# Optimization experiments

Hardware: AMD Instinct MI355X
Metric: run time of the kernel (lower is better)

The kernel has to match this reference:

```python
import jax, jax.numpy as jnp
import numpy as np

DIM = 256
HEADS = 8
WS = 7
MLP_HIDDEN = int(DIM * 2.0)
LN_EPS = 1e-5


def _ln(x, g, b):
    m = x.mean(-1, keepdims=True)
    v = ((x - m) ** 2).mean(-1, keepdims=True)
    return (x - m) / jnp.sqrt(v + LN_EPS) * g + b


def setup_inputs() -> dict:
    key = jax.random.key(0)
    ks = jax.random.split(key, 6)
    B, H, W, C = 32, 56, 56, DIM
    s = lambda k, shape: jax.random.normal(k, shape, jnp.float32) * 0.02
    return {
        "x": jax.random.normal(ks[0], (B, H * W, C), jnp.float32),
        "H": H,
        "W": W,
        "norm1_g": jnp.ones((C,), jnp.float32),
        "norm1_b": jnp.zeros((C,), jnp.float32),
        "in_proj_w": s(ks[1], (3 * C, C)),
        "in_proj_b": jnp.zeros((3 * C,), jnp.float32),
        "out_proj_w": s(ks[2], (C, C)),
        "out_proj_b": jnp.zeros((C,), jnp.float32),
        "norm2_g": jnp.ones((C,), jnp.float32),
        "norm2_b": jnp.zeros((C,), jnp.float32),
        "mlp_w1": s(ks[3], (MLP_HIDDEN, C)),
        "mlp_b1": jnp.zeros((MLP_HIDDEN,), jnp.float32),
        "mlp_w2": s(ks[4], (C, MLP_HIDDEN)),
        "mlp_b2": jnp.zeros((C,), jnp.float32),
    }


def reference(x, H, W, norm1_g, norm1_b, in_proj_w, in_proj_b, out_proj_w,
              out_proj_b, norm2_g, norm2_b, mlp_w1, mlp_b1, mlp_w2, mlp_b2):
    B, N, C = x.shape
    ws = WS
    shortcut = x

    h = _ln(x, norm1_g, norm1_b).reshape(B, H, W, C)  # channels-last (equiv. math)
    pad_h = (ws - H % ws) % ws
    pad_w = (ws - W % ws) % ws
    h = jnp.pad(h, ((0, 0), (0, pad_h), (0, pad_w), (0, 0)), mode="reflect")
    Hp, Wp = H + pad_h, W + pad_w
    nh, nw = Hp // ws, Wp // ws

    # window partition -> (B*nh*nw, ws*ws, C)
    h = h.reshape(B, nh, ws, nw, ws, C).transpose(0, 1, 3, 2, 4, 5)
    h = h.reshape(B * nh * nw, ws * ws, C)

    # torch nn.MultiheadAttention (batch_first), q=k=v=h
    hd = C // HEADS
    qkv = h @ in_proj_w.T + in_proj_b               # (Bw, L, 3C)
    q, k, v = jnp.split(qkv, 3, axis=-1)
    Bw, L, _ = q.shape
    q = q.reshape(Bw, L, HEADS, hd).transpose(0, 2, 1, 3)
    k = k.reshape(Bw, L, HEADS, hd).transpose(0, 2, 1, 3)
    v = v.reshape(Bw, L, HEADS, hd).transpose(0, 2, 1, 3)
    scores = jnp.einsum("bhqd,bhkd->bhqk", q, k) / jnp.sqrt(jnp.float32(hd))
    attn = jax.nn.softmax(scores, axis=-1)
    o = jnp.einsum("bhqk,bhkd->bhqd", attn, v)
    o = o.transpose(0, 2, 1, 3).reshape(Bw, L, C)
    o = o @ out_proj_w.T + out_proj_b

    # window merge, crop padding
    o = o.reshape(B, nh, nw, ws, ws, C).transpose(0, 1, 3, 2, 4, 5)
    o = o.reshape(B, Hp, Wp, C)[:, :H, :W, :].reshape(B, N, C)

    x = shortcut + o
    h2 = _ln(x, norm2_g, norm2_b)
    h2 = jax.nn.gelu(h2 @ mlp_w1.T + mlp_b1, approximate=False) @ mlp_w2.T + mlp_b2
    return x + h2
```

## Files before the change

kernel.cpp:

```cpp
#include <hip/hip_runtime.h>
#include <hip/hip_bf16.h>
#include <math.h>

#define NTOK 3136
#define C_ 256
#define HEADS_ 8
#define HD 32
#define WS_ 7
#define L_ 49
#define NWIN 2048
#define NWH 16384
#define M_ 100352
#define MLPH 512
#define WHSZ 2048

typedef __bf16 bf16x8 __attribute__((ext_vector_type(8)));
typedef float f32x4 __attribute__((ext_vector_type(4)));

__device__ __forceinline__ unsigned short f2bf(float f) {
    union { float f; unsigned u; } v; v.f = f;
    unsigned r = v.u + 0x7fffu + ((v.u >> 16) & 1u);
    return (unsigned short)(r >> 16);
}
__device__ __forceinline__ float bf2f(unsigned short s) {
    union { unsigned u; float f; } v; v.u = ((unsigned)s) << 16;
    return v.f;
}

__device__ __forceinline__ int t2rr(int t) {
    int win = t / L_;
    int l   = t - win * L_;
    int b_  = win >> 6, wh = (win >> 3) & 7, ww = win & 7;
    int ld7 = l / WS_;
    int y   = wh * WS_ + ld7;
    int xc  = ww * WS_ + (l - ld7 * WS_);
    return b_ * NTOK + y * 56 + xc;
}

template <int NBN>
__device__ __forceinline__ void xcd_decode(int nb, int& bm, int& bn) {
    int h = blockIdx.x;
    int fid = (h & 7) * (nb >> 3) + (h >> 3);
    int bmi = fid / NBN;
    bm = bmi * 128;
    bn = (fid - bmi * NBN) * 128;
}

__global__ __launch_bounds__(256) void cvt_kernel(
    const float* __restrict__ in, unsigned short* __restrict__ out, int n)
{
    int i = blockIdx.x * 256 + threadIdx.x;
    if (i < n) out[i] = f2bf(in[i]);
}

__global__ __launch_bounds__(256) void ln_kernel(
    const float* __restrict__ x, const float* __restrict__ gamma,
    const float* __restrict__ beta, unsigned short* __restrict__ out)
{
    int wave = threadIdx.x >> 6;
    int lane = threadIdx.x & 63;
    int p = blockIdx.x * 4 + wave;
    const float* row = x + (size_t)p * C_;
    float4 v = *(const float4*)(row + lane * 4);
    float s  = v.x + v.y + v.z + v.w;
    float ss = v.x * v.x + v.y * v.y + v.z * v.z + v.w * v.w;
    #pragma unroll
    for (int m = 1; m < 64; m <<= 1) {
        s  += __shfl_xor(s, m, 64);
        ss += __shfl_xor(ss, m, 64);
    }
    float mean = s * (1.0f / C_);
    float var  = ss * (1.0f / C_) - mean * mean;
    float inv  = rsqrtf(var + 1e-5f);
    float4 gv = *(const float4*)(gamma + lane * 4);
    float4 bv = *(const float4*)(beta + lane * 4);
    int b_ = p / NTOK, n = p - b_ * NTOK;
    int y = n / 56, xc = n - y * 56;
    int win = (b_ * 8 + y / WS_) * 8 + xc / WS_;
    int l   = (y % WS_) * WS_ + (xc % WS_);
    size_t orow = (size_t)(win * L_ + l) * C_;
    unsigned short o[4];
    o[0] = f2bf((v.x - mean) * inv * gv.x + bv.x);
    o[1] = f2bf((v.y - mean) * inv * gv.y + bv.y);
    o[2] = f2bf((v.z - mean) * inv * gv.z + bv.z);
    o[3] = f2bf((v.w - mean) * inv * gv.w + bv.w);
    *(uint2*)(out + orow + lane * 4) = *(const uint2*)o;
}

#define GBK 32

__device__ __forceinline__ void gload_lds16(const void* g, void* l) {
    __builtin_amdgcn_global_load_lds(
        (const __attribute__((address_space(1))) unsigned*)g,
        (__attribute__((address_space(3))) unsigned*)l, 16, 0, 0);
}

__global__ __launch_bounds__(256) void mgemm_qkv(
    const unsigned short* __restrict__ A, const unsigned short* __restrict__ W,
    const float* __restrict__ bias, unsigned short* __restrict__ qkv)
{
    __shared__ __align__(16) unsigned short As[4096];
    __shared__ __align__(16) unsigned short Bs[4096];

    int tid  = threadIdx.x;
    int w    = tid >> 6;
    int lane = tid & 63;
    int wr = w >> 1, wc = w & 1;
    int bm, bn;
    xcd_decode<6>(gridDim.x, bm, bn);
    int srow = lane >> 2;
    int scol = ((lane & 3) ^ ((lane >> 3) & 3)) * 8;
    int c = lane & 15, hi = lane >> 4;
    int hs = (hi ^ ((c >> 1) & 3)) * 8;

    f32x4 acc[4][4] = {};

    for (int k0 = 0; k0 < 256; k0 += GBK) {
        #pragma unroll
        for (int i = 0; i < 2; ++i) {
            int ra = w * 32 + i * 16;
            gload_lds16(A + (size_t)(bm + ra + srow) * 256 + k0 + scol, As + ra * GBK);
            gload_lds16(W + (size_t)(bn + ra + srow) * 256 + k0 + scol, Bs + ra * GBK);
        }
        __syncthreads();
        bf16x8 af[4], bf[4];
        #pragma unroll
        for (int mi = 0; mi < 4; ++mi)
            af[mi] = *(const bf16x8*)&As[(wr * 64 + mi * 16 + c) * GBK + hs];
        #pragma unroll
        for (int ni = 0; ni < 4; ++ni)
            bf[ni] = *(const bf16x8*)&Bs[(wc * 64 + ni * 16 + c) * GBK + hs];
        #pragma unroll
        for (int mi = 0; mi < 4; ++mi)
            #pragma unroll
            for (int ni = 0; ni < 4; ++ni)
                acc[mi][ni] = __builtin_amdgcn_mfma_f32_16x16x32_bf16(
                    af[mi], bf[ni], acc[mi][ni], 0, 0, 0);
        __syncthreads();
    }

    #pragma unroll
    for (int mi = 0; mi < 4; ++mi) {
        #pragma unroll
        for (int r = 0; r < 4; ++r) {
            int row = bm + wr * 64 + mi * 16 + hi * 4 + r;
            int win = row / L_, l = row - win * L_;
            #pragma unroll
            for (int ni = 0; ni < 4; ++ni) {
                int col = bn + wc * 64 + ni * 16 + c;
                float val = acc[mi][ni][r] + bias[col];
                int which = col >> 8;
                int head  = (col >> 5) & 7;
                int d     = col & 31;
                int wh = win * HEADS_ + head;
                size_t base = (size_t)which * ((size_t)NWH * WHSZ) + (size_t)wh * WHSZ;
                size_t off;
                if (which == 2)
                    off = base + (size_t)(((l >> 3) * HD + d) << 3) + (l & 7);
                else
                    off = base + (size_t)l * HD + d;
                qkv[off] = f2bf(val);
            }
        }
    }
}

__global__ __launch_bounds__(256) void mattn(
    const unsigned short* __restrict__ qkv, unsigned short* __restrict__ o_win)
{
    __shared__ __align__(16) unsigned short P_lds[4][64][72];
    int wave = threadIdx.x >> 6, lane = threadIdx.x & 63;
    int c = lane & 15, hi = lane >> 4;
    int wh = blockIdx.x * 4 + wave;
    int win = wh >> 3, head = wh & 7;
    const unsigned short* qb = qkv + (size_t)wh * WHSZ;
    const unsigned short* kb = qb + (size_t)NWH * WHSZ;
    const unsigned short* vb = kb + (size_t)NWH * WHSZ;

    bf16x8 af[4], bk[4];
    #pragma unroll
    for (int mi = 0; mi < 4; ++mi)
        af[mi] = *(const bf16x8*)(qb + (mi * 16 + c) * HD + hi * 8);
    #pragma unroll
    for (int ni = 0; ni < 4; ++ni)
        bk[ni] = *(const bf16x8*)(kb + (ni * 16 + c) * HD + hi * 8);

    f32x4 sacc[4][4] = {};
    #pragma unroll
    for (int mi = 0; mi < 4; ++mi)
        #pragma unroll
        for (int ni = 0; ni < 4; ++ni)
            sacc[mi][ni] = __builtin_amdgcn_mfma_f32_16x16x32_bf16(
                af[mi], bk[ni], sacc[mi][ni], 0, 0, 0);

    const float scale = 0.17677669529663687f;
    float inv_[4][4];
    #pragma unroll
    for (int mi = 0; mi < 4; ++mi) {
        #pragma unroll
        for (int r = 0; r < 4; ++r) {
            float sv[4];
            float m = -1e30f;
            #pragma unroll
            for (int ni = 0; ni < 4; ++ni) {
                float v = sacc[mi][ni][r] * scale;
                v = (ni * 16 + c < L_) ? v : -1e30f;
                sv[ni] = v;
                m = fmaxf(m, v);
            }
            #pragma unroll
            for (int msk = 1; msk < 16; msk <<= 1)
                m = fmaxf(m, __shfl_xor(m, msk, 64));
            float sum = 0.f;
            unsigned short pb[4];
            #pragma unroll
            for (int ni = 0; ni < 4; ++ni) {
                float p = __expf(sv[ni] - m);
                sum += p;
                pb[ni] = f2bf(p);
            }
            #pragma unroll
            for (int msk = 1; msk < 16; msk <<= 1)
                sum += __shfl_xor(sum, msk, 64);
            inv_[mi][r] = 1.0f / sum;
            int q = mi * 16 + hi * 4 + r;
            #pragma unroll
            for (int ni = 0; ni < 4; ++ni)
                P_lds[wave][q][ni * 16 + c] = pb[ni];
        }
    }

    f32x4 oacc[4][2] = {};
    #pragma unroll
    for (int ks = 0; ks < 2; ++ks) {
        bf16x8 pa[4], bv[2];
        #pragma unroll
        for (int mi = 0; mi < 4; ++mi)
            pa[mi] = *(const bf16x8*)&P_lds[wave][mi * 16 + c][ks * 32 + hi * 8];
        #pragma unroll
        for (int ni = 0; ni < 2; ++ni)
            bv[ni] = *(const bf16x8*)(vb + ((ks * 4 + hi) * HD + ni * 16 + c) * 8);
        #pragma unroll
        for (int mi = 0; mi < 4; ++mi)
            #pragma unroll
            for (int ni = 0; ni < 2; ++ni)
                oacc[mi][ni] = __builtin_amdgcn_mfma_f32_16x16x32_bf16(
                    pa[mi], bv[ni], oacc[mi][ni], 0, 0, 0);
    }

    #pragma unroll
    for (int mi = 0; mi < 4; ++mi) {
        #pragma unroll
        for (int r = 0; r < 4; ++r) {
            int q = mi * 16 + hi * 4 + r;
            if (q < L_) {
                size_t rowoff = ((size_t)(win * L_ + q)) * C_ + head * HD;
                float iv = inv_[mi][r];
                #pragma unroll
                for (int ni = 0; ni < 2; ++ni)
                    o_win[rowoff + ni * 16 + c] = f2bf(oacc[mi][ni][r] * iv);
            }
        }
    }
}

#define XS 260

__global__ __launch_bounds__(512) void mgemm_ln(
    const unsigned short* __restrict__ A, const unsigned short* __restrict__ W,
    const float* __restrict__ bias, const float* __restrict__ x,
    const float* __restrict__ g2, const float* __restrict__ b2,
    unsigned short* __restrict__ x1_out, unsigned short* __restrict__ ln_out)
{
    __shared__ __align__(16) unsigned short pool[128 * XS];
    unsigned short* As = pool;
    unsigned short* Bs = pool + 4096;

    int tid  = threadIdx.x;
    int w    = tid >> 6;
    int lane = tid & 63;
    int wr = w >> 2, wc = w & 3;
    int bm = blockIdx.x * 128;
    int srow = lane >> 2;
    int scol = ((lane & 3) ^ ((lane >> 3) & 3)) * 8;
    int c = lane & 15, hi = lane >> 4;
    int hs = (hi ^ ((c >> 1) & 3)) * 8;

    f32x4 acc[4][4] = {};

    for (int k0 = 0; k0 < 256; k0 += GBK) {
        gload_lds16(A + (size_t)(bm + w * 16 + srow) * 256 + k0 + scol,
                    As + (w * 16) * GBK);
        #pragma unroll
        for (int i = 0; i < 2; ++i) {
            int ra = w * 32 + i * 16;
            gload_lds16(W + (size_t)(ra + srow) * 256 + k0 + scol, Bs + ra * GBK);
        }
        __syncthreads();
        bf16x8 af[4], bf[4];
        #pragma unroll
        for (int mi = 0; mi < 4; ++mi)
            af[mi] = *(const bf16x8*)&As[(wr * 64 + mi * 16 + c) * GBK + hs];
        #pragma unroll
        for (int ni = 0; ni < 4; ++ni)
            bf[ni] = *(const bf16x8*)&Bs[(wc * 64 + ni * 16 + c) * GBK + hs];
        #pragma unroll
        for (int mi = 0; mi < 4; ++mi)
            #pragma unroll
            for (int ni = 0; ni < 4; ++ni)
                acc[mi][ni] = __builtin_amdgcn_mfma_f32_16x16x32_bf16(
                    af[mi], bf[ni], acc[mi][ni], 0, 0, 0);
        __syncthreads();
    }

    #pragma unroll
    for (int mi = 0; mi < 4; ++mi) {
        #pragma unroll
        for (int ni = 0; ni < 4; ++ni) {
            int colb = wc * 64 + ni * 16 + c;
            float bv = bias[colb];
            #pragma unroll
            for (int r = 0; r < 4; ++r)
                pool[(wr * 64 + mi * 16 + hi * 4 + r) * XS + colb] =
                    f2bf(acc[mi][ni][r] + bv);
        }
    }
    __syncthreads();

    float4 gv  = *(const float4*)(g2 + lane * 4);
    float4 bv2 = *(const float4*)(b2 + lane * 4);
    #pragma unroll 2
    for (int i = 0; i < 16; ++i) {
        int tl = w * 16 + i;
        int t = bm + tl;
        int rr = t2rr(t);
        float4 xv = *(const float4*)(x + (size_t)rr * C_ + lane * 4);
        uint2 ov = *(const uint2*)&pool[tl * XS + lane * 4];
        float x0 = xv.x + bf2f(ov.x & 0xffff);
        float x1 = xv.y + bf2f(ov.x >> 16);
        float x2 = xv.z + bf2f(ov.y & 0xffff);
        float x3 = xv.w + bf2f(ov.y >> 16);
        float s  = x0 + x1 + x2 + x3;
        float ss = x0 * x0 + x1 * x1 + x2 * x2 + x3 * x3;
        #pragma unroll
        for (int m = 1; m < 64; m <<= 1) {
            s  += __shfl_xor(s, m, 64);
            ss += __shfl_xor(ss, m, 64);
        }
        float mean = s * (1.0f / C_);
        float var  = ss * (1.0f / C_) - mean * mean;
        float inv  = rsqrtf(var + 1e-5f);
        uint2 xw, lw;
        xw.x = (unsigned)f2bf(x0) | ((unsigned)f2bf(x1) << 16);
        xw.y = (unsigned)f2bf(x2) | ((unsigned)f2bf(x3) << 16);
        float l0 = (x0 - mean) * inv * gv.x + bv2.x;
        float l1 = (x1 - mean) * inv * gv.y + bv2.y;
        float l2 = (x2 - mean) * inv * gv.z + bv2.z;
        float l3 = (x3 - mean) * inv * gv.w + bv2.w;
        lw.x = (unsigned)f2bf(l0) | ((unsigned)f2bf(l1) << 16);
        lw.y = (unsigned)f2bf(l2) | ((unsigned)f2bf(l3) << 16);
        *(uint2*)(x1_out + (size_t)t * C_ + lane * 4) = xw;
        *(uint2*)(ln_out + (size_t)t * C_ + lane * 4) = lw;
    }
}

#define TSS 136

__global__ __launch_bounds__(256) void mgemm_g(
    const unsigned short* __restrict__ A, const unsigned short* __restrict__ W,
    const float* __restrict__ bias, unsigned short* __restrict__ outp)
{
    __shared__ __align__(16) unsigned short pool[64 * TSS];
    unsigned short* As = pool;
    unsigned short* Bs = pool + 4096;
    unsigned short* Ts = pool;

    int tid  = threadIdx.x;
    int w    = tid >> 6;
    int lane = tid & 63;
    int wr = w >> 1, wc = w & 1;
    int bm, bn;
    xcd_decode<4>(gridDim.x, bm, bn);
    int srow = lane >> 2;
    int scol = ((lane & 3) ^ ((lane >> 3) & 3)) * 8;
    int c = lane & 15, hi = lane >> 4;
    int hs = (hi ^ ((c >> 1) & 3)) * 8;

    f32x4 acc[4][4] = {};

    for (int k0 = 0; k0 < 256; k0 += GBK) {
        #pragma unroll
        for (int i = 0; i < 2; ++i) {
            int ra = w * 32 + i * 16;
            gload_lds16(A + (size_t)(bm + ra + srow) * 256 + k0 + scol, As + ra * GBK);
            gload_lds16(W + (size_t)(bn + ra + srow) * 256 + k0 + scol, Bs + ra * GBK);
        }
        __syncthreads();
        bf16x8 af[4], bf[4];
        #pragma unroll
        for (int mi = 0; mi < 4; ++mi)
            af[mi] = *(const bf16x8*)&As[(wr * 64 + mi * 16 + c) * GBK + hs];
        #pragma unroll
        for (int ni = 0; ni < 4; ++ni)
            bf[ni] = *(const bf16x8*)&Bs[(wc * 64 + ni * 16 + c) * GBK + hs];
        #pragma unroll
        for (int mi = 0; mi < 4; ++mi)
            #pragma unroll
            for (int ni = 0; ni < 4; ++ni)
                acc[mi][ni] = __builtin_amdgcn_mfma_f32_16x16x32_bf16(
                    af[mi], bf[ni], acc[mi][ni], 0, 0, 0);
        __syncthreads();
    }

    #pragma unroll
    for (int ch = 0; ch < 2; ++ch) {
        if (wr == ch) {
            #pragma unroll
            for (int mi = 0; mi < 4; ++mi)
                #pragma unroll
                for (int ni = 0; ni < 4; ++ni) {
                    int colb = wc * 64 + ni * 16 + c;
                    float bv = bias[bn + colb];
                    #pragma unroll
                    for (int r = 0; r < 4; ++r) {
                        float v = acc[mi][ni][r] + bv;
                        float a = 1.5957691216f * (v + 0.044715f * v * v * v);
                        float g = v / (1.0f + __expf(-a));
                        Ts[(mi * 16 + hi * 4 + r) * TSS + colb] = f2bf(g);
                    }
                }
        }
        __syncthreads();
        #pragma unroll
        for (int it = 0; it < 4; ++it) {
            int id = it * 256 + tid;
            int row = id >> 4, cx = (id & 15) * 8;
            uint4 v = *(const uint4*)&Ts[row * TSS + cx];
            *(uint4*)&outp[(size_t)(bm + ch * 64 + row) * MLPH + bn + cx] = v;
        }
        __syncthreads();
    }
}

__global__ __launch_bounds__(256) void mgemm_out(
    const unsigned short* __restrict__ A, const unsigned short* __restrict__ W,
    const float* __restrict__ bias, const unsigned short* __restrict__ x1,
    float* __restrict__ dout)
{
    __shared__ __align__(16) unsigned short pool[8704];
    unsigned short* As = pool;
    unsigned short* Bs = pool + 4096;
    float* stg = (float*)pool;

    int tid  = threadIdx.x;
    int w    = tid >> 6;
    int lane = tid & 63;
    int wr = w >> 1, wc = w & 1;
    int bm, bn;
    xcd_decode<2>(gridDim.x, bm, bn);
    int srow = lane >> 2;
    int scol = ((lane & 3) ^ ((lane >> 3) & 3)) * 8;
    int c = lane & 15, hi = lane >> 4;
    int hs = (hi ^ ((c >> 1) & 3)) * 8;

    f32x4 acc[4][4] = {};

    for (int k0 = 0; k0 < 512; k0 += GBK) {
        #pragma unroll
        for (int i = 0; i < 2; ++i) {
            int ra = w * 32 + i * 16;
            gload_lds16(A + (size_t)(bm + ra + srow) * 512 + k0 + scol, As + ra * GBK);
            gload_lds16(W + (size_t)(bn + ra + srow) * 512 + k0 + scol, Bs + ra * GBK);
        }
        __syncthreads();
        bf16x8 af[4], bf[4];
        #pragma unroll
        for (int mi = 0; mi < 4; ++mi)
            af[mi] = *(const bf16x8*)&As[(wr * 64 + mi * 16 + c) * GBK + hs];
        #pragma unroll
        for (int ni = 0; ni < 4; ++ni)
            bf[ni] = *(const bf16x8*)&Bs[(wc * 64 + ni * 16 + c) * GBK + hs];
        #pragma unroll
        for (int mi = 0; mi < 4; ++mi)
            #pragma unroll
            for (int ni = 0; ni < 4; ++ni)
                acc[mi][ni] = __builtin_amdgcn_mfma_f32_16x16x32_bf16(
                    af[mi], bf[ni], acc[mi][ni], 0, 0, 0);
        __syncthreads();
    }

    #pragma unroll
    for (int c2 = 0; c2 < 4; ++c2) {
        if (wr == (c2 >> 1)) {
            int mi0 = (c2 & 1) * 2;
            #pragma unroll
            for (int mm = 0; mm < 2; ++mm) {
                #pragma unroll
                for (int ni = 0; ni < 4; ++ni) {
                    int colb = wc * 64 + ni * 16 + c;
                    float bv = bias[bn + colb];
                    #pragma unroll
                    for (int r = 0; r < 4; ++r)
                        stg[(mm * 16 + hi * 4 + r) * 132 + colb] =
                            acc[mi0 + mm][ni][r] + bv;
                }
            }
        }
        __syncthreads();
        #pragma unroll
        for (int i = 0; i < 4; ++i) {
            int lr = i * 8 + (tid >> 5);
            int t = bm + c2 * 32 + lr;
            int rr = t2rr(t);
            int col4 = (tid & 31) * 4;
            float4 v = *(const float4*)&stg[lr * 132 + col4];
            uint2 rv = *(const uint2*)&x1[(size_t)t * C_ + bn + col4];
            v.x += bf2f(rv.x & 0xffff);
            v.y += bf2f(rv.x >> 16);
            v.z += bf2f(rv.y & 0xffff);
            v.w += bf2f(rv.y >> 16);
            *(float4*)&dout[(size_t)rr * C_ + bn + col4] = v;
        }
        __syncthreads();
    }
}

extern "C" void kernel_launch(void* const* d_in, const int* in_sizes, int n_in,
                              void* d_out, int out_size, void* d_ws, size_t ws_size,
                              hipStream_t stream)
{
    (void)in_sizes; (void)n_in; (void)out_size; (void)ws_size;
    const float* x    = (const float*)d_in[0];
    const float* n1g  = (const float*)d_in[3];
    const float* n1b  = (const float*)d_in[4];
    const float* wqkv = (const float*)d_in[5];
    const float* bqkv = (const float*)d_in[6];
    const float* wout = (const float*)d_in[7];
    const float* bout = (const float*)d_in[8];
    const float* n2g  = (const float*)d_in[9];
    const float* n2b  = (const float*)d_in[10];
    const float* w1   = (const float*)d_in[11];
    const float* b1   = (const float*)d_in[12];
    const float* w2   = (const float*)d_in[13];
    const float* b2   = (const float*)d_in[14];
    float* out = (float*)d_out;

    unsigned short* bufA_bf = (unsigned short*)d_ws;
    unsigned short* qkv_bf  = bufA_bf + (size_t)M_ * C_;
    unsigned short* x1_bf   = qkv_bf + (size_t)3 * NWH * WHSZ;
    unsigned short* ln2_bf  = x1_bf + (size_t)M_ * C_;
    unsigned short* wqkv_bf = ln2_bf + (size_t)M_ * C_;
    unsigned short* wout_bf = wqkv_bf + 768 * 256;
    unsigned short* w1_bf   = wout_bf + 256 * 256;
    unsigned short* w2_bf   = w1_bf + 512 * 256;
    unsigned short* gelu    = qkv_bf;

    cvt_kernel<<<(768 * 256 + 255) / 256, 256, 0, stream>>>(wqkv, wqkv_bf, 768 * 256);
    cvt_kernel<<<(256 * 256 + 255) / 256, 256, 0, stream>>>(wout, wout_bf, 256 * 256);
    cvt_kernel<<<(512 * 256 + 255) / 256, 256, 0, stream>>>(w1, w1_bf, 512 * 256);
    cvt_kernel<<<(256 * 512 + 255) / 256, 256, 0, stream>>>(w2, w2_bf, 256 * 512);

    ln_kernel<<<M_ / 4, 256, 0, stream>>>(x, n1g, n1b, bufA_bf);

    mgemm_qkv<<<(M_ / 128) * 6, 256, 0, stream>>>(
        bufA_bf, wqkv_bf, bqkv, qkv_bf);

    mattn<<<NWH / 4, 256, 0, stream>>>(qkv_bf, bufA_bf);

    mgemm_ln<<<M_ / 128, 512, 0, stream>>>(
        bufA_bf, wout_bf, bout, x, n2g, n2b, x1_bf, ln2_bf);

    mgemm_g<<<(M_ / 128) * 4, 256, 0, stream>>>(ln2_bf, w1_bf, b1, gelu);

    mgemm_out<<<(M_ / 128) * 2, 256, 0, stream>>>(gelu, w2_bf, b2, x1_bf, out);
}
```

Baseline: 421.0 us.

## Double GEMM K-tile to 64 with new XOR swizzle and merge weight conversions

Raises the K step of all four bf16 MFMA GEMMs from 32 to 64. LDS tiles get an 8-way XOR swizzle, and each barrier pair now covers two MFMA sub-steps, halving the number of __syncthreads per GEMM. The four weight-conversion launches are folded into one vectorised kernel that relies on the weight buffers being contiguous in the workspace. In exchange each block uses more LDS, which may lower occupancy.

After: 401.5 us. -4.6%, faster.

```diff
diff --git a/kernel.cpp b/kernel.cpp
--- a/kernel.cpp
+++ b/kernel.cpp
@@ -46,11 +46,21 @@
     bn = (fid - bmi * NBN) * 128;
 }
 
-__global__ __launch_bounds__(256) void cvt_kernel(
-    const float* __restrict__ in, unsigned short* __restrict__ out, int n)
-{
-    int i = blockIdx.x * 256 + threadIdx.x;
-    if (i < n) out[i] = f2bf(in[i]);
+__global__ __launch_bounds__(256) void cvt4_kernel(
+    const float* __restrict__ a, const float* __restrict__ b,
+    const float* __restrict__ c2, const float* __restrict__ d,
+    unsigned short* __restrict__ out)
+{
+    int i = (blockIdx.x * 256 + threadIdx.x) * 4;
+    const float* src; int off;
+    if (i < 196608)      { src = a;  off = i; }
+    else if (i < 262144) { src = b;  off = i - 196608; }
+    else if (i < 393216) { src = c2; off = i - 262144; }
+    else                 { src = d;  off = i - 393216; }
+    float4 v = *(const float4*)(src + off);
+    unsigned short o[4];
+    o[0] = f2bf(v.x); o[1] = f2bf(v.y); o[2] = f2bf(v.z); o[3] = f2bf(v.w);
+    *(uint2*)(out + i) = *(const uint2*)o;
 }
 
 __global__ __launch_bounds__(256) void ln_kernel(
@@ -87,7 +97,7 @@
     *(uint2*)(out + orow + lane * 4) = *(const uint2*)o;
 }
 
-#define GBK 32
+#define GBK 64
 
 __device__ __forceinline__ void gload_lds16(const void* g, void* l) {
     __builtin_amdgcn_global_load_lds(
@@ -99,8 +109,8 @@
     const unsigned short* __restrict__ A, const unsigned short* __restrict__ W,
     const float* __restrict__ bias, unsigned short* __restrict__ qkv)
 {
-    __shared__ __align__(16) unsigned short As[4096];
-    __shared__ __align__(16) unsigned short Bs[4096];
+    __shared__ __align__(16) unsigned short As[8192];
+    __shared__ __align__(16) unsigned short Bs[8192];
 
     int tid  = threadIdx.x;
     int w    = tid >> 6;
@@ -108,34 +118,37 @@
     int wr = w >> 1, wc = w & 1;
     int bm, bn;
     xcd_decode<6>(gridDim.x, bm, bn);
-    int srow = lane >> 2;
-    int scol = ((lane & 3) ^ ((lane >> 3) & 3)) * 8;
+    int srow8 = lane >> 3;
+    int scol  = ((lane & 7) ^ srow8) * 8;
     int c = lane & 15, hi = lane >> 4;
-    int hs = (hi ^ ((c >> 1) & 3)) * 8;
 
     f32x4 acc[4][4] = {};
 
     for (int k0 = 0; k0 < 256; k0 += GBK) {
         #pragma unroll
-        for (int i = 0; i < 2; ++i) {
-            int ra = w * 32 + i * 16;
-            gload_lds16(A + (size_t)(bm + ra + srow) * 256 + k0 + scol, As + ra * GBK);
-            gload_lds16(W + (size_t)(bn + ra + srow) * 256 + k0 + scol, Bs + ra * GBK);
-        }
-        __syncthreads();
-        bf16x8 af[4], bf[4];
-        #pragma unroll
-        for (int mi = 0; mi < 4; ++mi)
-            af[mi] = *(const bf16x8*)&As[(wr * 64 + mi * 16 + c) * GBK + hs];
-        #pragma unroll
-        for (int ni = 0; ni < 4; ++ni)
-            bf[ni] = *(const bf16x8*)&Bs[(wc * 64 + ni * 16 + c) * GBK + hs];
-        #pragma unroll
-        for (int mi = 0; mi < 4; ++mi)
+        for (int it = 0; it < 4; ++it) {
+            int rb = it * 32 + w * 8;
+            gload_lds16(A + (size_t)(bm + rb + srow8) * 256 + k0 + scol, As + rb * 64);
+            gload_lds16(W + (size_t)(bn + rb + srow8) * 256 + k0 + scol, Bs + rb * 64);
+        }
+        __syncthreads();
+        #pragma unroll
+        for (int kk = 0; kk < 2; ++kk) {
+            bf16x8 af[4], bf[4];
+            int hs = ((kk * 4 + hi) ^ (c & 7)) * 8;
+            #pragma unroll
+            for (int mi = 0; mi < 4; ++mi)
+                af[mi] = *(const bf16x8*)&As[(wr * 64 + mi * 16 + c) * 64 + hs];
             #pragma unroll
             for (int ni = 0; ni < 4; ++ni)
-                acc[mi][ni] = __builtin_amdgcn_mfma_f32_16x16x32_bf16(
-                    af[mi], bf[ni], acc[mi][ni], 0, 0, 0);
+                bf[ni] = *(const bf16x8*)&Bs[(wc * 64 + ni * 16 + c) * 64 + hs];
+            #pragma unroll
+            for (int mi = 0; mi < 4; ++mi)
+                #pragma unroll
+                for (int ni = 0; ni < 4; ++ni)
+                    acc[mi][ni] = __builtin_amdgcn_mfma_f32_16x16x32_bf16(
+                        af[mi], bf[ni], acc[mi][ni], 0, 0, 0);
+        }
         __syncthreads();
     }
 
@@ -274,42 +287,48 @@
 {
     __shared__ __align__(16) unsigned short pool[128 * XS];
     unsigned short* As = pool;
-    unsigned short* Bs = pool + 4096;
+    unsigned short* Bs = pool + 8192;
 
     int tid  = threadIdx.x;
     int w    = tid >> 6;
     int lane = tid & 63;
     int wr = w >> 2, wc = w & 3;
     int bm = blockIdx.x * 128;
-    int srow = lane >> 2;
-    int scol = ((lane & 3) ^ ((lane >> 3) & 3)) * 8;
+    int srow8 = lane >> 3;
+    int scol  = ((lane & 7) ^ srow8) * 8;
     int c = lane & 15, hi = lane >> 4;
-    int hs = (hi ^ ((c >> 1) & 3)) * 8;
 
     f32x4 acc[4][4] = {};
 
     for (int k0 = 0; k0 < 256; k0 += GBK) {
-        gload_lds16(A + (size_t)(bm + w * 16 + srow) * 256 + k0 + scol,
-                    As + (w * 16) * GBK);
-        #pragma unroll
-        for (int i = 0; i < 2; ++i) {
-            int ra = w * 32 + i * 16;
-            gload_lds16(W + (size_t)(ra + srow) * 256 + k0 + scol, Bs + ra * GBK);
-        }
-        __syncthreads();
-        bf16x8 af[4], bf[4];
-        #pragma unroll
-        for (int mi = 0; mi < 4; ++mi)
-            af[mi] = *(const bf16x8*)&As[(wr * 64 + mi * 16 + c) * GBK + hs];
-        #pragma unroll
-        for (int ni = 0; ni < 4; ++ni)
-            bf[ni] = *(const bf16x8*)&Bs[(wc * 64 + ni * 16 + c) * GBK + hs];
-        #pragma unroll
-        for (int mi = 0; mi < 4; ++mi)
+        #pragma unroll
+        for (int it = 0; it < 2; ++it) {
+            int rb = it * 64 + w * 8;
+            gload_lds16(A + (size_t)(bm + rb + srow8) * 256 + k0 + scol, As + rb * 64);
+        }
+        #pragma unroll
+        for (int it = 0; it < 4; ++it) {
+            int rb = it * 64 + w * 8;
+            gload_lds16(W + (size_t)(rb + srow8) * 256 + k0 + scol, Bs + rb * 64);
+        }
+        __syncthreads();
+        #pragma unroll
+        for (int kk = 0; kk < 2; ++kk) {
+            bf16x8 af[4], bf[4];
+            int hs = ((kk * 4 + hi) ^ (c & 7)) * 8;
+            #pragma unroll
+            for (int mi = 0; mi < 4; ++mi)
+                af[mi] = *(const bf16x8*)&As[(wr * 64 + mi * 16 + c) * 64 + hs];
             #pragma unroll
             for (int ni = 0; ni < 4; ++ni)
-                acc[mi][ni] = __builtin_amdgcn_mfma_f32_16x16x32_bf16(
-                    af[mi], bf[ni], acc[mi][ni], 0, 0, 0);
+                bf[ni] = *(const bf16x8*)&Bs[(wc * 64 + ni * 16 + c) * 64 + hs];
+            #pragma unroll
+            for (int mi = 0; mi < 4; ++mi)
+                #pragma unroll
+                for (int ni = 0; ni < 4; ++ni)
+                    acc[mi][ni] = __builtin_amdgcn_mfma_f32_16x16x32_bf16(
+                        af[mi], bf[ni], acc[mi][ni], 0, 0, 0);
+        }
         __syncthreads();
     }
 
@@ -370,9 +389,9 @@
     const unsigned short* __restrict__ A, const unsigned short* __restrict__ W,
     const float* __restrict__ bias, unsigned short* __restrict__ outp)
 {
-    __shared__ __align__(16) unsigned short pool[64 * TSS];
+    __shared__ __align__(16) unsigned short pool[16384];
     unsigned short* As = pool;
-    unsigned short* Bs = pool + 4096;
+    unsigned short* Bs = pool + 8192;
     unsigned short* Ts = pool;
 
     int tid  = threadIdx.x;
@@ -381,34 +400,37 @@
     int wr = w >> 1, wc = w & 1;
     int bm, bn;
     xcd_decode<4>(gridDim.x, bm, bn);
-    int srow = lane >> 2;
-    int scol = ((lane & 3) ^ ((lane >> 3) & 3)) * 8;
+    int srow8 = lane >> 3;
+    int scol  = ((lane & 7) ^ srow8) * 8;
     int c = lane & 15, hi = lane >> 4;
-    int hs = (hi ^ ((c >> 1) & 3)) * 8;
 
     f32x4 acc[4][4] = {};
 
     for (int k0 = 0; k0 < 256; k0 += GBK) {
         #pragma unroll
-        for (int i = 0; i < 2; ++i) {
-            int ra = w * 32 + i * 16;
-            gload_lds16(A + (size_t)(bm + ra + srow) * 256 + k0 + scol, As + ra * GBK);
-            gload_lds16(W + (size_t)(bn + ra + srow) * 256 + k0 + scol, Bs + ra * GBK);
-        }
-        __syncthreads();
-        bf16x8 af[4], bf[4];
-        #pragma unroll
-        for (int mi = 0; mi < 4; ++mi)
-            af[mi] = *(const bf16x8*)&As[(wr * 64 + mi * 16 + c) * GBK + hs];
-        #pragma unroll
-        for (int ni = 0; ni < 4; ++ni)
-            bf[ni] = *(const bf16x8*)&Bs[(wc * 64 + ni * 16 + c) * GBK + hs];
-        #pragma unroll
-        for (int mi = 0; mi < 4; ++mi)
+        for (int it = 0; it < 4; ++it) {
+            int rb = it * 32 + w * 8;
+            gload_lds16(A + (size_t)(bm + rb + srow8) * 256 + k0 + scol, As + rb * 64);
+            gload_lds16(W + (size_t)(bn + rb + srow8) * 256 + k0 + scol, Bs + rb * 64);
+        }
+        __syncthreads();
+        #pragma unroll
+        for (int kk = 0; kk < 2; ++kk) {
+            bf16x8 af[4], bf[4];
+            int hs = ((kk * 4 + hi) ^ (c & 7)) * 8;
+            #pragma unroll
+            for (int mi = 0; mi < 4; ++mi)
+                af[mi] = *(const bf16x8*)&As[(wr * 64 + mi * 16 + c) * 64 + hs];
             #pragma unroll
             for (int ni = 0; ni < 4; ++ni)
-                acc[mi][ni] = __builtin_amdgcn_mfma_f32_16x16x32_bf16(
-                    af[mi], bf[ni], acc[mi][ni], 0, 0, 0);
+                bf[ni] = *(const bf16x8*)&Bs[(wc * 64 + ni * 16 + c) * 64 + hs];
+            #pragma unroll
+            for (int mi = 0; mi < 4; ++mi)
+                #pragma unroll
+                for (int ni = 0; ni < 4; ++ni)
+                    acc[mi][ni] = __builtin_amdgcn_mfma_f32_16x16x32_bf16(
+                        af[mi], bf[ni], acc[mi][ni], 0, 0, 0);
+        }
         __syncthreads();
     }
 
@@ -447,9 +469,9 @@
     const float* __restrict__ bias, const unsigned short* __restrict__ x1,
     float* __restrict__ dout)
 {
-    __shared__ __align__(16) unsigned short pool[8704];
+    __shared__ __align__(16) unsigned short pool[16384];
     unsigned short* As = pool;
-    unsigned short* Bs = pool + 4096;
+    unsigned short* Bs = pool + 8192;
     float* stg = (float*)pool;
 
     int tid  = threadIdx.x;
@@ -458,34 +480,37 @@
     int wr = w >> 1, wc = w & 1;
     int bm, bn;
     xcd_decode<2>(gridDim.x, bm, bn);
-    int srow = lane >> 2;
-    int scol = ((lane & 3) ^ ((lane >> 3) & 3)) * 8;
+    int srow8 = lane >> 3;
+    int scol  = ((lane & 7) ^ srow8) * 8;
     int c = lane & 15, hi = lane >> 4;
-    int hs = (hi ^ ((c >> 1) & 3)) * 8;
 
     f32x4 acc[4][4] = {};
 
     for (int k0 = 0; k0 < 512; k0 += GBK) {
         #pragma unroll
-        for (int i = 0; i < 2; ++i) {
-            int ra = w * 32 + i * 16;
-            gload_lds16(A + (size_t)(bm + ra + srow) * 512 + k0 + scol, As + ra * GBK);
-            gload_lds16(W + (size_t)(bn + ra + srow) * 512 + k0 + scol, Bs + ra * GBK);
-        }
-        __syncthreads();
-        bf16x8 af[4], bf[4];
-        #pragma unroll
-        for (int mi = 0; mi < 4; ++mi)
-            af[mi] = *(const bf16x8*)&As[(wr * 64 + mi * 16 + c) * GBK + hs];
-        #pragma unroll
-        for (int ni = 0; ni < 4; ++ni)
-            bf[ni] = *(const bf16x8*)&Bs[(wc * 64 + ni * 16 + c) * GBK + hs];
-        #pragma unroll
-        for (int mi = 0; mi < 4; ++mi)
+        for (int it = 0; it < 4; ++it) {
+            int rb = it * 32 + w * 8;
+            gload_lds16(A + (size_t)(bm + rb + srow8) * 512 + k0 + scol, As + rb * 64);
+            gload_lds16(W + (size_t)(bn + rb + srow8) * 512 + k0 + scol, Bs + rb * 64);
+        }
+        __syncthreads();
+        #pragma unroll
+        for (int kk = 0; kk < 2; ++kk) {
+            bf16x8 af[4], bf[4];
+            int hs = ((kk * 4 + hi) ^ (c & 7)) * 8;
+            #pragma unroll
+            for (int mi = 0; mi < 4; ++mi)
+                af[mi] = *(const bf16x8*)&As[(wr * 64 + mi * 16 + c) * 64 + hs];
             #pragma unroll
             for (int ni = 0; ni < 4; ++ni)
-                acc[mi][ni] = __builtin_amdgcn_mfma_f32_16x16x32_bf16(
-                    af[mi], bf[ni], acc[mi][ni], 0, 0, 0);
+                bf[ni] = *(const bf16x8*)&Bs[(wc * 64 + ni * 16 + c) * 64 + hs];
+            #pragma unroll
+            for (int mi = 0; mi < 4; ++mi)
+                #pragma unroll
+                for (int ni = 0; ni < 4; ++ni)
+                    acc[mi][ni] = __builtin_amdgcn_mfma_f32_16x16x32_bf16(
+                        af[mi], bf[ni], acc[mi][ni], 0, 0, 0);
+        }
         __syncthreads();
     }
 
@@ -555,10 +580,7 @@
     unsigned short* w2_bf   = w1_bf + 512 * 256;
     unsigned short* gelu    = qkv_bf;
 
-    cvt_kernel<<<(768 * 256 + 255) / 256, 256, 0, stream>>>(wqkv, wqkv_bf, 768 * 256);
-    cvt_kernel<<<(256 * 256 + 255) / 256, 256, 0, stream>>>(wout, wout_bf, 256 * 256);
-    cvt_kernel<<<(512 * 256 + 255) / 256, 256, 0, stream>>>(w1, w1_bf, 512 * 256);
-    cvt_kernel<<<(256 * 512 + 255) / 256, 256, 0, stream>>>(w2, w2_bf, 256 * 512);
+    cvt4_kernel<<<512, 256, 0, stream>>>(wqkv, wout, w1, w2, wqkv_bf);
 
     ln_kernel<<<M_ / 4, 256, 0, stream>>>(x, n1g, n1b, bufA_bf);
 
```
